# Kernel optimization log

Hardware: AMD Instinct MI355X
Metric: run time of the kernel (lower is better)

## Reference

```python
import jax, jax.numpy as jnp
import numpy as np

N_HEAD, D_MODEL, D_K, D_V = 16, 1024, 64, 64
B, LQ, LK = 4, 2048, 2048


def setup_inputs() -> dict:
    key = jax.random.key(0)
    ks = jax.random.split(key, 10)
    q = jax.random.normal(ks[0], (B, LQ, D_MODEL), dtype=jnp.float32)
    k = jax.random.normal(ks[1], (B, LK, D_MODEL), dtype=jnp.float32)
    v = jax.random.normal(ks[2], (B, LK, D_MODEL), dtype=jnp.float32)
    mask = jax.random.randint(ks[3], (B, LQ, LK), 0, 2).astype(bool)
    s_qk = np.sqrt(2.0 / (D_MODEL + D_K)).astype(np.float32)
    s_v = np.sqrt(2.0 / (D_MODEL + D_V)).astype(np.float32)
    w_qs = jax.random.normal(ks[4], (D_MODEL, N_HEAD * D_K), dtype=jnp.float32) * s_qk
    w_ks = jax.random.normal(ks[5], (D_MODEL, N_HEAD * D_K), dtype=jnp.float32) * s_qk
    w_vs = jax.random.normal(ks[6], (D_MODEL, N_HEAD * D_V), dtype=jnp.float32) * s_v
    b_qs = jnp.zeros((N_HEAD * D_K,), jnp.float32)
    b_ks = jnp.zeros((N_HEAD * D_K,), jnp.float32)
    b_vs = jnp.zeros((N_HEAD * D_V,), jnp.float32)
    fc_w = jax.random.normal(ks[7], (N_HEAD * D_V, D_MODEL), dtype=jnp.float32) * np.sqrt(2.0 / (N_HEAD * D_V + D_MODEL)).astype(np.float32)
    fc_b = jnp.zeros((D_MODEL,), jnp.float32)
    return {"q": q, "k": k, "v": v, "mask": mask,
            "w_qs": w_qs, "b_qs": b_qs, "w_ks": w_ks, "b_ks": b_ks,
            "w_vs": w_vs, "b_vs": b_vs, "fc_w": fc_w, "fc_b": fc_b}


def mha(q, k, v, mask, w_qs, b_qs, w_ks, b_ks, w_vs, b_vs, fc_w, fc_b):
    residual = q
    b, lq, _ = q.shape
    lk = k.shape[1]
    # project and split heads: [b, h, len, d]
    qh = (q @ w_qs + b_qs).reshape(b, lq, N_HEAD, D_K).transpose(0, 2, 1, 3)
    kh = (k @ w_ks + b_ks).reshape(b, lk, N_HEAD, D_K).transpose(0, 2, 1, 3)
    vh = (v @ w_vs + b_vs).reshape(b, lk, N_HEAD, D_V).transpose(0, 2, 1, 3)
    temperature = jnp.asarray(D_K ** 0.5, qh.dtype)
    attn = jnp.einsum('bhqd,bhkd->bhqk', qh, kh) / temperature
    attn = jnp.where(mask[:, None, :, :], -jnp.inf, attn)
    attn = jax.nn.softmax(attn, axis=-1)  # dropout is identity in eval
    out = jnp.einsum('bhqk,bhkd->bhqd', attn, vh)
    out = out.transpose(0, 2, 1, 3).reshape(b, lq, N_HEAD * D_V)
    out = out @ fc_w + fc_b
    return out + residual, attn


def reference(q, k, v, mask, w_qs, b_qs, w_ks, b_ks, w_vs, b_vs, fc_w, fc_b):
    return mha(q, k, v, mask, w_qs, b_qs, w_ks, b_ks, w_vs, b_vs, fc_w, fc_b)
```

## Files before the change

kernel.cpp:

```cpp
#include <hip/hip_runtime.h>
#include <cstdint>
#include <cstddef>

typedef unsigned short u16;
typedef unsigned long long u64;
typedef __bf16 bf16x8 __attribute__((ext_vector_type(8)));
typedef float floatx4 __attribute__((ext_vector_type(4)));
typedef u16 u16x8 __attribute__((ext_vector_type(8)));

#define NHEAD 16
#define DHEAD 64
#define BATCH 4
#define SEQ 2048
#define DMODEL 1024

__device__ __forceinline__ u16 f2b(float f) {
  union { float f; unsigned u; } x; x.f = f;
  unsigned r = x.u + 0x7fffu + ((x.u >> 16) & 1u);
  return (u16)(r >> 16);
}

__device__ __forceinline__ floatx4 mfma16(bf16x8 a, bf16x8 b, floatx4 c) {
  return __builtin_amdgcn_mfma_f32_16x16x32_bf16(a, b, c, 0, 0, 0);
}

__global__ __launch_bounds__(256) void wtrans(const float* __restrict__ w,
                                              u16* __restrict__ wt) {
  __shared__ u16 tile[64 * 68];
  const int t = threadIdx.x;
  const int d0 = blockIdx.x * 64, c0 = blockIdx.y * 64;
#pragma unroll
  for (int s = 0; s < 4; ++s) {
    int dd = (t >> 4) + s * 16;
    int cc = (t & 15) * 4;
    float4 v = *(const float4*)(w + (size_t)(d0 + dd) * DMODEL + c0 + cc);
    u16* p = &tile[dd * 68 + cc];
    p[0] = f2b(v.x); p[1] = f2b(v.y); p[2] = f2b(v.z); p[3] = f2b(v.w);
  }
  __syncthreads();
#pragma unroll
  for (int s = 0; s < 2; ++s) {
    int cc = (t >> 3) + s * 32;
    int dd = (t & 7) * 8;
    u16x8 rv;
#pragma unroll
    for (int j = 0; j < 8; ++j) rv[j] = tile[(dd + j) * 68 + cc];
    *(u16x8*)(wt + (size_t)(c0 + cc) * DMODEL + d0 + dd) = rv;
  }
}

__global__ __launch_bounds__(256) void maskpack(const void* __restrict__ maskp,
                                                u64* __restrict__ mpk) {
  const int t = threadIdx.x;
  unsigned mw = ((const unsigned*)maskp)[t & 63];
  const bool bytemask = __ballot(mw > 1u) != 0ull;
  const int rl = t >> 5, kt = t & 31;
  const int row = blockIdx.x * 8 + rl;
  const int b = blockIdx.y;
  const size_t eoff = ((size_t)b * SEQ + row) * SEQ + (size_t)kt * 64;
  u64 bits = 0;
  if (bytemask) {
    const uint4* p = (const uint4*)((const unsigned char*)maskp + eoff);
#pragma unroll
    for (int j = 0; j < 4; ++j) {
      uint4 v = p[j];
      unsigned wd[4] = {v.x, v.y, v.z, v.w};
#pragma unroll
      for (int q = 0; q < 4; ++q)
#pragma unroll
        for (int by = 0; by < 4; ++by)
          bits |= (u64)(((wd[q] >> (8 * by)) & 0xffu) ? 1u : 0u)
                  << (j * 16 + q * 4 + by);
    }
  } else {
    const uint4* p = (const uint4*)((const unsigned*)maskp + eoff);
#pragma unroll
    for (int j = 0; j < 16; ++j) {
      uint4 v = p[j];
      bits |= (u64)(v.x ? 1 : 0) << (j * 4 + 0);
      bits |= (u64)(v.y ? 1 : 0) << (j * 4 + 1);
      bits |= (u64)(v.z ? 1 : 0) << (j * 4 + 2);
      bits |= (u64)(v.w ? 1 : 0) << (j * 4 + 3);
    }
  }
  mpk[((size_t)b * SEQ + row) * 32 + kt] = bits;
}

__global__ __launch_bounds__(256) void gemm128(
    const float* __restrict__ Af, const u16* __restrict__ Ab,
    const u16* __restrict__ WT, const float* __restrict__ bias,
    u16* __restrict__ outb, float* __restrict__ outf,
    const float* __restrict__ resid, int mode) {
  __shared__ __align__(16) u16 sm[2 * 128 * 72];
  u16* sA = sm;
  u16* sB = sm + 128 * 72;
  const int t = threadIdx.x;
  const int w = t >> 6, lane = t & 63, quad = lane >> 4, ln = lane & 15;
  const int Mb = blockIdx.x * 128, Nb = blockIdx.y * 128;
  const int wr = (w >> 1) * 64, wc = (w & 1) * 64;
  floatx4 acc[4][4] = {};
#pragma unroll 1
  for (int kc = 0; kc < 16; ++kc) {
    const int k0 = kc * 64;
    __syncthreads();
    if (mode == 2) {
#pragma unroll
      for (int s = 0; s < 4; ++s) {
        int r = (t >> 3) + s * 32, off = (t & 7) * 8;
        *(u16x8*)(&sA[r * 72 + off]) =
            *(const u16x8*)(Ab + (size_t)(Mb + r) * DMODEL + k0 + off);
      }
    } else {
#pragma unroll
      for (int s = 0; s < 8; ++s) {
        int r = (t >> 4) + s * 16, c = (t & 15) * 4;
        float4 v = *(const float4*)(Af + (size_t)(Mb + r) * DMODEL + k0 + c);
        u16* p = &sA[r * 72 + c];
        p[0] = f2b(v.x); p[1] = f2b(v.y); p[2] = f2b(v.z); p[3] = f2b(v.w);
      }
    }
#pragma unroll
    for (int s = 0; s < 4; ++s) {
      int r = (t >> 3) + s * 32, off = (t & 7) * 8;
      *(u16x8*)(&sB[r * 72 + off]) =
          *(const u16x8*)(WT + (size_t)(Nb + r) * DMODEL + k0 + off);
    }
    __syncthreads();
#pragma unroll
    for (int ks = 0; ks < 2; ++ks) {
      bf16x8 af[4], bfr[4];
#pragma unroll
      for (int m = 0; m < 4; ++m)
        af[m] = *(const bf16x8*)(&sA[(wr + m * 16 + ln) * 72 + quad * 8 + ks * 32]);
#pragma unroll
      for (int n = 0; n < 4; ++n)
        bfr[n] = *(const bf16x8*)(&sB[(wc + n * 16 + ln) * 72 + quad * 8 + ks * 32]);
#pragma unroll
      for (int m = 0; m < 4; ++m)
#pragma unroll
        for (int n = 0; n < 4; ++n)
          acc[m][n] = mfma16(af[m], bfr[n], acc[m][n]);
    }
  }
  float bv[4];
#pragma unroll
  for (int n = 0; n < 4; ++n) bv[n] = bias[Nb + wc + n * 16 + ln];

  if (mode == 0) {
#pragma unroll
    for (int m = 0; m < 4; ++m)
#pragma unroll
      for (int n = 0; n < 4; ++n)
#pragma unroll
        for (int rr = 0; rr < 4; ++rr) {
          int row = Mb + wr + m * 16 + quad * 4 + rr;
          int c = Nb + wc + n * 16 + ln;
          int bi = row >> 11, lq = row & 2047, h = c >> 6, dk = c & 63;
          outb[(((size_t)bi * NHEAD + h) * SEQ + lq) * DHEAD + dk] =
              f2b(acc[m][n][rr] + bv[n]);
        }
  } else if (mode == 2) {
#pragma unroll
    for (int m = 0; m < 4; ++m)
#pragma unroll
      for (int n = 0; n < 4; ++n)
#pragma unroll
        for (int rr = 0; rr < 4; ++rr) {
          int row = Mb + wr + m * 16 + quad * 4 + rr;
          int c = Nb + wc + n * 16 + ln;
          size_t idx = (size_t)row * DMODEL + c;
          outf[idx] = acc[m][n][rr] + bv[n] + resid[idx];
        }
  } else {
    __syncthreads();
    u16* tb = sm;
#pragma unroll
    for (int m = 0; m < 4; ++m)
#pragma unroll
      for (int n = 0; n < 4; ++n)
#pragma unroll
        for (int rr = 0; rr < 4; ++rr) {
          int rl = wr + m * 16 + quad * 4 + rr;
          int cl = wc + n * 16 + ln;
          tb[rl * 132 + cl] = f2b(acc[m][n][rr] + bv[n]);
        }
    __syncthreads();
    for (int s = 0; s < 64; ++s) {
      int flat = s * 256 + t;
      int cl = flat >> 7, lkl = flat & 127;
      int c = Nb + cl, h = c >> 6, dk = c & 63;
      int lk = Mb + lkl, bi = lk >> 11, lkq = lk & 2047;
      outb[(((size_t)bi * NHEAD + h) * DHEAD + dk) * SEQ + lkq] =
          tb[lkl * 132 + cl];
    }
  }
}

__global__ __launch_bounds__(256, 4) void attn2(
    const u16* __restrict__ qh, const u16* __restrict__ kh,
    const u16* __restrict__ vT, const u64* __restrict__ mpk,
    float* __restrict__ attn_o, u16* __restrict__ ao) {
  __shared__ __align__(16) u16 ps[4][16 * 72];
  const int t = threadIdx.x;
  const int w = t >> 6, lane = t & 63, quad = lane >> 4, ln = lane & 15;
  const int qt = blockIdx.x, bh = blockIdx.y;
  const int b = bh >> 4;
  const int q0 = qt * 64 + w * 16;
  const float SC = 0.18033688011112042f;

  bf16x8 qf[2];
  {
    const u16* qbase = qh + ((size_t)bh * SEQ + q0 + ln) * DHEAD + quad * 8;
    qf[0] = *(const bf16x8*)(qbase);
    qf[1] = *(const bf16x8*)(qbase + 32);
  }
  const u16* kbase = kh + (size_t)bh * SEQ * DHEAD;
  const u16* vbase = vT + (size_t)bh * DHEAD * SEQ;
  const u64* mrow = mpk + ((size_t)b * SEQ + q0 + quad * 4) * 32;

  float lsum[4] = {0.f, 0.f, 0.f, 0.f};
#pragma unroll 1
  for (int kt = 0; kt < 32; ++kt) {
    u64 mv[4];
#pragma unroll
    for (int rr = 0; rr < 4; ++rr) mv[rr] = mrow[rr * 32 + kt];
    floatx4 sc4[4] = {};
#pragma unroll
    for (int kss = 0; kss < 2; ++kss)
#pragma unroll
      for (int n = 0; n < 4; ++n) {
        bf16x8 kf = *(const bf16x8*)(kbase + (size_t)(kt * 64 + n * 16 + ln) * DHEAD +
                                     quad * 8 + kss * 32);
        sc4[n] = mfma16(qf[kss], kf, sc4[n]);
      }
#pragma unroll
    for (int rr = 0; rr < 4; ++rr) {
#pragma unroll
      for (int n = 0; n < 4; ++n) {
        float e = exp2f(sc4[n][rr] * SC);
        bool blk = (mv[rr] >> (n * 16 + ln)) & 1;
        lsum[rr] += blk ? 0.f : e;
      }
    }
  }
  float il[4];
#pragma unroll
  for (int rr = 0; rr < 4; ++rr) {
    float s = lsum[rr];
#pragma unroll
    for (int o = 1; o < 16; o <<= 1) s += __shfl_xor(s, o);
    il[rr] = 1.0f / s;
  }

  floatx4 oa[4] = {};
  u16* myps = ps[w];
  float* pout = attn_o + (size_t)bh * SEQ * SEQ;
#pragma unroll 1
  for (int kt = 0; kt < 32; ++kt) {
    u64 mv[4];
#pragma unroll
    for (int rr = 0; rr < 4; ++rr) mv[rr] = mrow[rr * 32 + kt];
    floatx4 sc4[4] = {};
#pragma unroll
    for (int kss = 0; kss < 2; ++kss)
#pragma unroll
      for (int n = 0; n < 4; ++n) {
        bf16x8 kf = *(const bf16x8*)(kbase + (size_t)(kt * 64 + n * 16 + ln) * DHEAD +
                                     quad * 8 + kss * 32);
        sc4[n] = mfma16(qf[kss], kf, sc4[n]);
      }
#pragma unroll
    for (int rr = 0; rr < 4; ++rr) {
      int qrow = q0 + quad * 4 + rr;
#pragma unroll
      for (int n = 0; n < 4; ++n) {
        bool blk = (mv[rr] >> (n * 16 + ln)) & 1;
        float pn = blk ? 0.f : exp2f(sc4[n][rr] * SC) * il[rr];
        __builtin_nontemporal_store(
            pn, &pout[(size_t)qrow * SEQ + kt * 64 + n * 16 + ln]);
        myps[(quad * 4 + rr) * 72 + n * 16 + ln] = f2b(pn);
      }
    }
#pragma unroll
    for (int kss = 0; kss < 2; ++kss) {
      bf16x8 pa = *(const bf16x8*)(&myps[ln * 72 + quad * 8 + kss * 32]);
#pragma unroll
      for (int n = 0; n < 4; ++n) {
        bf16x8 vf = *(const bf16x8*)(vbase + (size_t)(n * 16 + ln) * SEQ +
                                     kt * 64 + quad * 8 + kss * 32);
        oa[n] = mfma16(pa, vf, oa[n]);
      }
    }
  }
#pragma unroll
  for (int n = 0; n < 4; ++n)
#pragma unroll
    for (int rr = 0; rr < 4; ++rr) {
      int row = q0 + quad * 4 + rr;
      ao[((size_t)b * SEQ + row) * DMODEL + (bh & 15) * DHEAD + n * 16 + ln] =
          f2b(oa[n][rr]);
    }
}

extern "C" void kernel_launch(void* const* d_in, const int* in_sizes, int n_in,
                              void* d_out, int out_size, void* d_ws,
                              size_t ws_size, hipStream_t stream) {
  (void)in_sizes; (void)n_in; (void)out_size; (void)ws_size;
  const float* q = (const float*)d_in[0];
  const float* k = (const float*)d_in[1];
  const float* v = (const float*)d_in[2];
  const void* mask = d_in[3];
  const float* w_qs = (const float*)d_in[4];
  const float* b_qs = (const float*)d_in[5];
  const float* w_ks = (const float*)d_in[6];
  const float* b_ks = (const float*)d_in[7];
  const float* w_vs = (const float*)d_in[8];
  const float* b_vs = (const float*)d_in[9];
  const float* fc_w = (const float*)d_in[10];
  const float* fc_b = (const float*)d_in[11];

  char* ws = (char*)d_ws;
  const size_t WSZ = (size_t)DMODEL * DMODEL * 2;
  const size_t HSZ = (size_t)BATCH * NHEAD * SEQ * DHEAD * 2;
  u16* wqT = (u16*)(ws + 0 * WSZ);
  u16* wkT = (u16*)(ws + 1 * WSZ);
  u16* wvT = (u16*)(ws + 2 * WSZ);
  u16* fcT = (u16*)(ws + 3 * WSZ);
  u16* qh = (u16*)(ws + 4 * WSZ);
  u16* kh = (u16*)(ws + 4 * WSZ + HSZ);
  u16* vhT = (u16*)(ws + 4 * WSZ + 2 * HSZ);
  u16* ao = (u16*)(ws + 4 * WSZ + 3 * HSZ);
  u64* mpk = (u64*)(ws + 4 * WSZ + 4 * HSZ);

  float* out0 = (float*)d_out;
  float* attn = out0 + (size_t)BATCH * SEQ * DMODEL;

  dim3 tgrid(16, 16);
  wtrans<<<tgrid, 256, 0, stream>>>(w_qs, wqT);
  wtrans<<<tgrid, 256, 0, stream>>>(w_ks, wkT);
  wtrans<<<tgrid, 256, 0, stream>>>(w_vs, wvT);
  wtrans<<<tgrid, 256, 0, stream>>>(fc_w, fcT);

  maskpack<<<dim3(SEQ / 8, BATCH), 256, 0, stream>>>(mask, mpk);

  dim3 ggrid(64, 8);
  gemm128<<<ggrid, 256, 0, stream>>>(q, nullptr, wqT, b_qs, qh, nullptr, nullptr, 0);
  gemm128<<<ggrid, 256, 0, stream>>>(k, nullptr, wkT, b_ks, kh, nullptr, nullptr, 0);
  gemm128<<<ggrid, 256, 0, stream>>>(v, nullptr, wvT, b_vs, vhT, nullptr, nullptr, 1);

  attn2<<<dim3(32, 64), 256, 0, stream>>>(qh, kh, vhT, mpk, attn, ao);

  gemm128<<<ggrid, 256, 0, stream>>>(nullptr, ao, fcT, fc_b, nullptr, out0, q, 2);
}
```

Measured before the change: 1.923 ms.

## Pre-convert inputs to bf16, shrink GEMM tiles, transpose attention MFMA for vector stores

Adds a standalone fp32-to-bf16 conversion kernel so the projection GEMMs read bf16 A operands, and halves the GEMM M tile to 64 rows with more blocks and a higher occupancy bound. The softmax scale is folded into the Q projection epilogue. The attention kernel swaps MFMA operand order so each lane owns one query row. That allows float4 nontemporal stores of the attention matrix, packed LDS writes, a single-row mask load and a cheaper row-sum reduction. It also hoists V loads ahead of the stores and remaps blocks so heads group by XCD. The extra conversion pass adds memory traffic, and the occupancy bound on the attention kernel is lowered to 3.

```diff
diff --git a/kernel.cpp b/kernel.cpp
--- a/kernel.cpp
+++ b/kernel.cpp
@@ -7,6 +7,7 @@
 typedef __bf16 bf16x8 __attribute__((ext_vector_type(8)));
 typedef float floatx4 __attribute__((ext_vector_type(4)));
 typedef u16 u16x8 __attribute__((ext_vector_type(8)));
+typedef u16 u16x4 __attribute__((ext_vector_type(4)));
 
 #define NHEAD 16
 #define DHEAD 64
@@ -22,6 +23,16 @@
 
 __device__ __forceinline__ floatx4 mfma16(bf16x8 a, bf16x8 b, floatx4 c) {
   return __builtin_amdgcn_mfma_f32_16x16x32_bf16(a, b, c, 0, 0, 0);
+}
+
+__global__ __launch_bounds__(256) void tobf16(const float* __restrict__ in,
+                                              u16* __restrict__ out) {
+  size_t i = ((size_t)blockIdx.x * 256 + threadIdx.x) * 8;
+  float4 a = *(const float4*)(in + i);
+  float4 b = *(const float4*)(in + i + 4);
+  u16x8 r = {f2b(a.x), f2b(a.y), f2b(a.z), f2b(a.w),
+             f2b(b.x), f2b(b.y), f2b(b.z), f2b(b.w)};
+  *(u16x8*)(out + i) = r;
 }
 
 __global__ __launch_bounds__(256) void wtrans(const float* __restrict__ w,
@@ -86,38 +97,28 @@
   mpk[((size_t)b * SEQ + row) * 32 + kt] = bits;
 }
 
-__global__ __launch_bounds__(256) void gemm128(
-    const float* __restrict__ Af, const u16* __restrict__ Ab,
-    const u16* __restrict__ WT, const float* __restrict__ bias,
-    u16* __restrict__ outb, float* __restrict__ outf,
-    const float* __restrict__ resid, int mode) {
-  __shared__ __align__(16) u16 sm[2 * 128 * 72];
+__global__ __launch_bounds__(256, 4) void gemm64(
+    const u16* __restrict__ A, const u16* __restrict__ WT,
+    const float* __restrict__ bias, u16* __restrict__ outb,
+    float* __restrict__ outf, const float* __restrict__ resid,
+    float oscale, int mode) {
+  __shared__ __align__(16) u16 sm[64 * 72 + 128 * 72];
   u16* sA = sm;
-  u16* sB = sm + 128 * 72;
+  u16* sB = sm + 64 * 72;
   const int t = threadIdx.x;
   const int w = t >> 6, lane = t & 63, quad = lane >> 4, ln = lane & 15;
-  const int Mb = blockIdx.x * 128, Nb = blockIdx.y * 128;
-  const int wr = (w >> 1) * 64, wc = (w & 1) * 64;
-  floatx4 acc[4][4] = {};
+  const int Mb = blockIdx.x * 64, Nb = blockIdx.y * 128;
+  const int wr = (w >> 1) * 32, wc = (w & 1) * 64;
+  floatx4 acc[2][4] = {};
 #pragma unroll 1
   for (int kc = 0; kc < 16; ++kc) {
     const int k0 = kc * 64;
     __syncthreads();
-    if (mode == 2) {
-#pragma unroll
-      for (int s = 0; s < 4; ++s) {
-        int r = (t >> 3) + s * 32, off = (t & 7) * 8;
-        *(u16x8*)(&sA[r * 72 + off]) =
-            *(const u16x8*)(Ab + (size_t)(Mb + r) * DMODEL + k0 + off);
-      }
-    } else {
-#pragma unroll
-      for (int s = 0; s < 8; ++s) {
-        int r = (t >> 4) + s * 16, c = (t & 15) * 4;
-        float4 v = *(const float4*)(Af + (size_t)(Mb + r) * DMODEL + k0 + c);
-        u16* p = &sA[r * 72 + c];
-        p[0] = f2b(v.x); p[1] = f2b(v.y); p[2] = f2b(v.z); p[3] = f2b(v.w);
-      }
+#pragma unroll
+    for (int s = 0; s < 2; ++s) {
+      int r = (t >> 3) + s * 32, off = (t & 7) * 8;
+      *(u16x8*)(&sA[r * 72 + off]) =
+          *(const u16x8*)(A + (size_t)(Mb + r) * DMODEL + k0 + off);
     }
 #pragma unroll
     for (int s = 0; s < 4; ++s) {
@@ -128,15 +129,15 @@
     __syncthreads();
 #pragma unroll
     for (int ks = 0; ks < 2; ++ks) {
-      bf16x8 af[4], bfr[4];
-#pragma unroll
-      for (int m = 0; m < 4; ++m)
+      bf16x8 af[2], bfr[4];
+#pragma unroll
+      for (int m = 0; m < 2; ++m)
         af[m] = *(const bf16x8*)(&sA[(wr + m * 16 + ln) * 72 + quad * 8 + ks * 32]);
 #pragma unroll
       for (int n = 0; n < 4; ++n)
         bfr[n] = *(const bf16x8*)(&sB[(wc + n * 16 + ln) * 72 + quad * 8 + ks * 32]);
 #pragma unroll
-      for (int m = 0; m < 4; ++m)
+      for (int m = 0; m < 2; ++m)
 #pragma unroll
         for (int n = 0; n < 4; ++n)
           acc[m][n] = mfma16(af[m], bfr[n], acc[m][n]);
@@ -148,7 +149,7 @@
 
   if (mode == 0) {
 #pragma unroll
-    for (int m = 0; m < 4; ++m)
+    for (int m = 0; m < 2; ++m)
 #pragma unroll
       for (int n = 0; n < 4; ++n)
 #pragma unroll
@@ -157,11 +158,11 @@
           int c = Nb + wc + n * 16 + ln;
           int bi = row >> 11, lq = row & 2047, h = c >> 6, dk = c & 63;
           outb[(((size_t)bi * NHEAD + h) * SEQ + lq) * DHEAD + dk] =
-              f2b(acc[m][n][rr] + bv[n]);
+              f2b((acc[m][n][rr] + bv[n]) * oscale);
         }
   } else if (mode == 2) {
 #pragma unroll
-    for (int m = 0; m < 4; ++m)
+    for (int m = 0; m < 2; ++m)
 #pragma unroll
       for (int n = 0; n < 4; ++n)
 #pragma unroll
@@ -175,19 +176,19 @@
     __syncthreads();
     u16* tb = sm;
 #pragma unroll
-    for (int m = 0; m < 4; ++m)
+    for (int m = 0; m < 2; ++m)
 #pragma unroll
       for (int n = 0; n < 4; ++n)
 #pragma unroll
         for (int rr = 0; rr < 4; ++rr) {
           int rl = wr + m * 16 + quad * 4 + rr;
           int cl = wc + n * 16 + ln;
-          tb[rl * 132 + cl] = f2b(acc[m][n][rr] + bv[n]);
+          tb[rl * 132 + cl] = f2b((acc[m][n][rr] + bv[n]) * oscale);
         }
     __syncthreads();
-    for (int s = 0; s < 64; ++s) {
+    for (int s = 0; s < 32; ++s) {
       int flat = s * 256 + t;
-      int cl = flat >> 7, lkl = flat & 127;
+      int cl = flat >> 6, lkl = flat & 63;
       int c = Nb + cl, h = c >> 6, dk = c & 63;
       int lk = Mb + lkl, bi = lk >> 11, lkq = lk & 2047;
       outb[(((size_t)bi * NHEAD + h) * DHEAD + dk) * SEQ + lkq] =
@@ -196,17 +197,18 @@
   }
 }
 
-__global__ __launch_bounds__(256, 4) void attn2(
+__global__ __launch_bounds__(256, 3) void attn3(
     const u16* __restrict__ qh, const u16* __restrict__ kh,
     const u16* __restrict__ vT, const u64* __restrict__ mpk,
     float* __restrict__ attn_o, u16* __restrict__ ao) {
   __shared__ __align__(16) u16 ps[4][16 * 72];
   const int t = threadIdx.x;
   const int w = t >> 6, lane = t & 63, quad = lane >> 4, ln = lane & 15;
-  const int qt = blockIdx.x, bh = blockIdx.y;
+  const int id = blockIdx.x;
+  const int xcd = id & 7, j = id >> 3;
+  const int bh = xcd * 8 + (j >> 5), qt = j & 31;
   const int b = bh >> 4;
   const int q0 = qt * 64 + w * 16;
-  const float SC = 0.18033688011112042f;
 
   bf16x8 qf[2];
   {
@@ -216,14 +218,12 @@
   }
   const u16* kbase = kh + (size_t)bh * SEQ * DHEAD;
   const u16* vbase = vT + (size_t)bh * DHEAD * SEQ;
-  const u64* mrow = mpk + ((size_t)b * SEQ + q0 + quad * 4) * 32;
-
-  float lsum[4] = {0.f, 0.f, 0.f, 0.f};
-#pragma unroll 1
+  const u64* mrow = mpk + ((size_t)b * SEQ + q0 + ln) * 32;
+
+  float lsum = 0.f;
+#pragma unroll 2
   for (int kt = 0; kt < 32; ++kt) {
-    u64 mv[4];
-#pragma unroll
-    for (int rr = 0; rr < 4; ++rr) mv[rr] = mrow[rr * 32 + kt];
+    u64 mv = mrow[kt];
     floatx4 sc4[4] = {};
 #pragma unroll
     for (int kss = 0; kss < 2; ++kss)
@@ -231,35 +231,28 @@
       for (int n = 0; n < 4; ++n) {
         bf16x8 kf = *(const bf16x8*)(kbase + (size_t)(kt * 64 + n * 16 + ln) * DHEAD +
                                      quad * 8 + kss * 32);
-        sc4[n] = mfma16(qf[kss], kf, sc4[n]);
+        sc4[n] = mfma16(kf, qf[kss], sc4[n]);
       }
 #pragma unroll
-    for (int rr = 0; rr < 4; ++rr) {
-#pragma unroll
-      for (int n = 0; n < 4; ++n) {
-        float e = exp2f(sc4[n][rr] * SC);
-        bool blk = (mv[rr] >> (n * 16 + ln)) & 1;
-        lsum[rr] += blk ? 0.f : e;
+    for (int n = 0; n < 4; ++n) {
+      unsigned bits = (unsigned)(mv >> (n * 16 + quad * 4)) & 0xFu;
+#pragma unroll
+      for (int rr = 0; rr < 4; ++rr) {
+        float e = exp2f(sc4[n][rr]);
+        lsum += ((bits >> rr) & 1u) ? 0.f : e;
       }
     }
   }
-  float il[4];
-#pragma unroll
-  for (int rr = 0; rr < 4; ++rr) {
-    float s = lsum[rr];
-#pragma unroll
-    for (int o = 1; o < 16; o <<= 1) s += __shfl_xor(s, o);
-    il[rr] = 1.0f / s;
-  }
+  lsum += __shfl_xor(lsum, 16);
+  lsum += __shfl_xor(lsum, 32);
+  const float il = 1.0f / lsum;
 
   floatx4 oa[4] = {};
   u16* myps = ps[w];
-  float* pout = attn_o + (size_t)bh * SEQ * SEQ;
+  float* prow = attn_o + (size_t)bh * SEQ * SEQ + (size_t)(q0 + ln) * SEQ + quad * 4;
 #pragma unroll 1
   for (int kt = 0; kt < 32; ++kt) {
-    u64 mv[4];
-#pragma unroll
-    for (int rr = 0; rr < 4; ++rr) mv[rr] = mrow[rr * 32 + kt];
+    u64 mv = mrow[kt];
     floatx4 sc4[4] = {};
 #pragma unroll
     for (int kss = 0; kss < 2; ++kss)
@@ -267,29 +260,37 @@
       for (int n = 0; n < 4; ++n) {
         bf16x8 kf = *(const bf16x8*)(kbase + (size_t)(kt * 64 + n * 16 + ln) * DHEAD +
                                      quad * 8 + kss * 32);
-        sc4[n] = mfma16(qf[kss], kf, sc4[n]);
+        sc4[n] = mfma16(kf, qf[kss], sc4[n]);
       }
-#pragma unroll
-    for (int rr = 0; rr < 4; ++rr) {
-      int qrow = q0 + quad * 4 + rr;
-#pragma unroll
-      for (int n = 0; n < 4; ++n) {
-        bool blk = (mv[rr] >> (n * 16 + ln)) & 1;
-        float pn = blk ? 0.f : exp2f(sc4[n][rr] * SC) * il[rr];
-        __builtin_nontemporal_store(
-            pn, &pout[(size_t)qrow * SEQ + kt * 64 + n * 16 + ln]);
-        myps[(quad * 4 + rr) * 72 + n * 16 + ln] = f2b(pn);
+    floatx4 pf[4];
+#pragma unroll
+    for (int n = 0; n < 4; ++n) {
+      unsigned bits = (unsigned)(mv >> (n * 16 + quad * 4)) & 0xFu;
+#pragma unroll
+      for (int rr = 0; rr < 4; ++rr) {
+        float e = exp2f(sc4[n][rr]) * il;
+        pf[n][rr] = ((bits >> rr) & 1u) ? 0.f : e;
       }
-    }
+      u16x4 pk = {f2b(pf[n][0]), f2b(pf[n][1]), f2b(pf[n][2]), f2b(pf[n][3])};
+      *(u16x4*)(&myps[ln * 72 + n * 16 + quad * 4]) = pk;
+    }
+    bf16x8 vf[8];
+#pragma unroll
+    for (int kss = 0; kss < 2; ++kss)
+#pragma unroll
+      for (int n = 0; n < 4; ++n)
+        vf[kss * 4 + n] = *(const bf16x8*)(vbase + (size_t)(n * 16 + ln) * SEQ +
+                                           kt * 64 + quad * 8 + kss * 32);
+#pragma unroll
+    for (int n = 0; n < 4; ++n)
+      __builtin_nontemporal_store(pf[n],
+                                  (floatx4*)(prow + (size_t)kt * 64 + n * 16));
 #pragma unroll
     for (int kss = 0; kss < 2; ++kss) {
       bf16x8 pa = *(const bf16x8*)(&myps[ln * 72 + quad * 8 + kss * 32]);
 #pragma unroll
-      for (int n = 0; n < 4; ++n) {
-        bf16x8 vf = *(const bf16x8*)(vbase + (size_t)(n * 16 + ln) * SEQ +
-                                     kt * 64 + quad * 8 + kss * 32);
-        oa[n] = mfma16(pa, vf, oa[n]);
-      }
+      for (int n = 0; n < 4; ++n)
+        oa[n] = mfma16(pa, vf[kss * 4 + n], oa[n]);
     }
   }
 #pragma unroll
@@ -331,9 +332,12 @@
   u16* vhT = (u16*)(ws + 4 * WSZ + 2 * HSZ);
   u16* ao = (u16*)(ws + 4 * WSZ + 3 * HSZ);
   u64* mpk = (u64*)(ws + 4 * WSZ + 4 * HSZ);
+  u16* cvt = (u16*)(ws + 4 * WSZ + 4 * HSZ + (size_t)2 * 1024 * 1024);
 
   float* out0 = (float*)d_out;
   float* attn = out0 + (size_t)BATCH * SEQ * DMODEL;
+
+  const float SC = 0.18033688011112042f;
 
   dim3 tgrid(16, 16);
   wtrans<<<tgrid, 256, 0, stream>>>(w_qs, wqT);
@@ -343,12 +347,15 @@
 
   maskpack<<<dim3(SEQ / 8, BATCH), 256, 0, stream>>>(mask, mpk);
 
-  dim3 ggrid(64, 8);
-  gemm128<<<ggrid, 256, 0, stream>>>(q, nullptr, wqT, b_qs, qh, nullptr, nullptr, 0);
-  gemm128<<<ggrid, 256, 0, stream>>>(k, nullptr, wkT, b_ks, kh, nullptr, nullptr, 0);
-  gemm128<<<ggrid, 256, 0, stream>>>(v, nullptr, wvT, b_vs, vhT, nullptr, nullptr, 1);
-
-  attn2<<<dim3(32, 64), 256, 0, stream>>>(qh, kh, vhT, mpk, attn, ao);
-
-  gemm128<<<ggrid, 256, 0, stream>>>(nullptr, ao, fcT, fc_b, nullptr, out0, q, 2);
-}
+  dim3 ggrid(128, 8);
+  tobf16<<<4096, 256, 0, stream>>>(q, cvt);
+  gemm64<<<ggrid, 256, 0, stream>>>(cvt, wqT, b_qs, qh, nullptr, nullptr, SC, 0);
+  tobf16<<<4096, 256, 0, stream>>>(k, cvt);
+  gemm64<<<ggrid, 256, 0, stream>>>(cvt, wkT, b_ks, kh, nullptr, nullptr, 1.0f, 0);
+  tobf16<<<4096, 256, 0, stream>>>(v, cvt);
+  gemm64<<<ggrid, 256, 0, stream>>>(cvt, wvT, b_vs, vhT, nullptr, nullptr, 1.0f, 1);
+
+  attn3<<<dim3(2048), 256, 0, stream>>>(qh, kh, vhT, mpk, attn, ao);
+
+  gemm64<<<ggrid, 256, 0, stream>>>(ao, fcT, fc_b, nullptr, out0, q, 1.0f, 2);
+}
```

New measurement: 1.963 ms. 2.0% more time.
